# Kernel optimization log

Measured on AMD Instinct MI355X. Metric: run time of the kernel, lower is better.

The kernel has to match this reference:

```python
import jax, jax.numpy as jnp
import numpy as np

NUM_HEADS = 16

def setup_inputs() -> dict:
    key = jax.random.key(0)
    ks = jax.random.split(key, 6)
    B, N, E = 2, 2048, 2048
    QK, V, M = 2048, 2048, 4096
    x = jax.random.normal(ks[0], (B, N, E), dtype=jnp.float32)
    Wq = jax.random.normal(ks[1], (QK, E), dtype=jnp.float32) * 0.02
    k_weight = jax.random.normal(ks[2], (M, QK), dtype=jnp.float32) * 0.05
    v_weight = jax.random.normal(ks[3], (M, V), dtype=jnp.float32) * 0.05
    Wg = jax.random.normal(ks[4], (V, E), dtype=jnp.float32) * 0.02
    Wout = jax.random.normal(ks[5], (E, V), dtype=jnp.float32) * 0.02
    return {"x": x, "Wq": Wq, "k_weight": k_weight, "v_weight": v_weight, "Wg": Wg, "Wout": Wout}

def reference(x, Wq, k_weight, v_weight, Wg, Wout):
    H = NUM_HEADS
    B, N, E = x.shape
    M = k_weight.shape[0]
    # q: [B, N, QK] -> [B, H, N, dk]
    q = jnp.einsum('bne,fe->bnf', x, Wq)
    dk = q.shape[-1] // H
    q = q.reshape(B, N, H, dk).transpose(0, 2, 1, 3)
    # k: [M, QK] -> [H, M, dk]; v: [M, V] -> [H, M, dv]
    k = k_weight.reshape(M, H, dk).transpose(1, 0, 2)
    dv = v_weight.shape[1] // H
    v = v_weight.reshape(M, H, dv).transpose(1, 0, 2)
    scale = jnp.asarray(dk, x.dtype) ** 0.5  # use_scale == 1
    k = k * scale
    v = v * scale
    # non-softmax attention over fixed memory
    energy = jax.nn.silu(jnp.einsum('bhnd,hmd->bhnm', q, k))  # [B,H,N,M]
    out = jnp.einsum('bhnm,hmd->bhnd', energy, v)  # [B,H,N,dv]
    out = out.transpose(0, 2, 1, 3).reshape(B, N, H * dv)
    # output gate (silu)
    gate = jax.nn.silu(jnp.einsum('bne,ve->bnv', x, Wg))
    out = out * gate
    return jnp.einsum('bnv,ev->bne', out, Wout)
```

## Files before the change

### kernel.cpp

```cpp
#include <hip/hip_runtime.h>

typedef __bf16 bf16;
typedef __bf16 bf16x4 __attribute__((ext_vector_type(4)));
typedef __bf16 bf16x8 __attribute__((ext_vector_type(8)));
typedef float f32x4 __attribute__((ext_vector_type(4)));

#define MFMA(a, b, c) __builtin_amdgcn_mfma_f32_16x16x32_bf16(a, b, c, 0, 0, 0)

__device__ __forceinline__ float fast_silu(float x) {
  float e = __builtin_amdgcn_exp2f(x * -1.4426950408889634f);
  return x * __builtin_amdgcn_rcpf(1.f + e);
}

__device__ __forceinline__ void gload_lds16(const void* g, void* l) {
  __builtin_amdgcn_global_load_lds(
      (const __attribute__((address_space(1))) void*)g,
      (__attribute__((address_space(3))) void*)l, 16, 0, 0);
}

__global__ __launch_bounds__(256) void cvt_bf16(const float* __restrict__ in,
                                                bf16* __restrict__ out, int n) {
  int i = (blockIdx.x * 256 + threadIdx.x) * 4;
  if (i >= n) return;
  float4 v = *(const float4*)(in + i);
  bf16x4 o = {(bf16)v.x, (bf16)v.y, (bf16)v.z, (bf16)v.w};
  *(bf16x4*)(out + i) = o;
}

__global__ __launch_bounds__(256) void transpose_v_cvt(const float* __restrict__ v,
                                                       bf16* __restrict__ vt) {
  __shared__ bf16 T[64 * 72];
  const int m0 = blockIdx.x * 64, c0 = blockIdx.y * 64;
  const int tid = threadIdx.x;
  const int tr = tid >> 3;
  const int tc = (tid & 7) << 3;
#pragma unroll
  for (int it = 0; it < 2; it++) {
    int r = tr + it * 32;
    const float* src = v + (long)(m0 + r) * 2048 + c0 + tc;
    float4 a = *(const float4*)src;
    float4 b = *(const float4*)(src + 4);
    bf16x8 t = {(bf16)a.x, (bf16)a.y, (bf16)a.z, (bf16)a.w,
                (bf16)b.x, (bf16)b.y, (bf16)b.z, (bf16)b.w};
    *(bf16x8*)&T[r * 72 + tc] = t;
  }
  __syncthreads();
#pragma unroll
  for (int it = 0; it < 2; it++) {
    int c = tr + it * 32;
    bf16x8 o;
#pragma unroll
    for (int j = 0; j < 8; j++) o[j] = T[(tc + j) * 72 + c];
    *(bf16x8*)(vt + (long)(c0 + c) * 4096 + m0 + tc) = o;
  }
}

template <int MODE, int BM>
__global__ __launch_bounds__(512, 2) void gemm256(const bf16* __restrict__ A,
                                                  const bf16* __restrict__ B,
                                                  const bf16* __restrict__ B2,
                                                  bf16* __restrict__ C1,
                                                  bf16* __restrict__ C2,
                                                  float* __restrict__ Cf, int K, int N) {
  constexpr int MR = BM / 32;
  constexpr int MR2 = MR / 2;
  constexpr int AL = BM / 64;
  __shared__ bf16 As[3][BM * 64];
  __shared__ bf16 Bs[2][256 * 64];

  const int tid = threadIdx.x, wave = tid >> 6, lane = tid & 63;
  const int wr = wave >> 2, wc = wave & 3;
  const int quad = lane >> 4, fr = lane & 15;

  const int id2 = (blockIdx.x & 7) * 32 + (blockIdx.x >> 3);
  const int gx = (MODE == 3) ? (id2 >> 4) : (id2 >> 5);
  const int gy = (MODE == 3) ? (id2 & 15) : (id2 & 31);
  const bool gsel = (MODE == 3) && (gx >= 8);
  const bf16* Bm = gsel ? B2 : B;
  const long bM = (long)gy * BM;
  const long bN = (long)((MODE == 3) ? (gx & 7) : gx) * 256;

  f32x4 acc[MR][4] = {};

  const int srow = tid >> 3;
  const int sblk = (tid & 7) ^ (srow & 7);
  const bf16* Ag = A + (bM + srow) * (long)K + (sblk << 3);
  const bf16* Bg = Bm + (bN + srow) * (long)K + (sblk << 3);
  const int sdst = srow * 64 + ((tid & 7) << 3);

  auto stA = [&](int kt, int sb) {
#pragma unroll
    for (int i = 0; i < AL; i++)
      gload_lds16(Ag + (long)i * 64 * K + kt * 64, &As[sb][sdst + i * 64 * 64]);
  };
  auto stB = [&](int kt, int sb) {
#pragma unroll
    for (int i = 0; i < 4; i++)
      gload_lds16(Bg + (long)i * 64 * K + kt * 64, &Bs[sb][sdst + i * 64 * 64]);
  };
  auto rdA = [&](int ab, int mi, int kk) {
    int row = wr * (BM / 2) + mi * 16 + fr;
    return *(const bf16x8*)&As[ab][row * 64 + (((kk * 4 + quad) ^ (fr & 7)) << 3)];
  };
  auto rdB = [&](int bb, int ni, int kk) {
    int row = wc * 64 + ni * 16 + fr;
    return *(const bf16x8*)&Bs[bb][row * 64 + (((kk * 4 + quad) ^ (fr & 7)) << 3)];
  };

  const int NT = K >> 6;
  stB(0, 0);
  stA(0, 0);
  stA(NT > 1 ? 1 : 0, 1);
  if constexpr (AL == 4)
    asm volatile("s_waitcnt vmcnt(4)" ::: "memory");
  else
    asm volatile("s_waitcnt vmcnt(2)" ::: "memory");
  __builtin_amdgcn_s_barrier();

  for (int kt = 0; kt < NT; ++kt) {
    const int ra = kt % 3, rb = kt & 1;
    bf16x8 bfv[4][2], ah[MR2][2];

    stB(kt + 1 < NT ? kt + 1 : NT - 1, (kt + 1) & 1);
    stA(kt + 2 < NT ? kt + 2 : NT - 1, (kt + 2) % 3);
#pragma unroll
    for (int ni = 0; ni < 4; ni++)
#pragma unroll
      for (int kk = 0; kk < 2; kk++) bfv[ni][kk] = rdB(rb, ni, kk);
#pragma unroll
    for (int mi = 0; mi < MR2; mi++)
#pragma unroll
      for (int kk = 0; kk < 2; kk++) ah[mi][kk] = rdA(ra, mi, kk);
    __builtin_amdgcn_s_barrier();
    __builtin_amdgcn_s_setprio(1);
#pragma unroll
    for (int mi = 0; mi < MR2; mi++)
#pragma unroll
      for (int ni = 0; ni < 2; ni++)
#pragma unroll
        for (int kk = 0; kk < 2; kk++) acc[mi][ni] = MFMA(ah[mi][kk], bfv[ni][kk], acc[mi][ni]);
    __builtin_amdgcn_s_setprio(0);
    __builtin_amdgcn_s_barrier();

    __builtin_amdgcn_s_setprio(1);
#pragma unroll
    for (int mi = 0; mi < MR2; mi++)
#pragma unroll
      for (int ni = 2; ni < 4; ni++)
#pragma unroll
        for (int kk = 0; kk < 2; kk++) acc[mi][ni] = MFMA(ah[mi][kk], bfv[ni][kk], acc[mi][ni]);
    __builtin_amdgcn_s_setprio(0);
    __builtin_amdgcn_s_barrier();

#pragma unroll
    for (int mi = 0; mi < MR2; mi++)
#pragma unroll
      for (int kk = 0; kk < 2; kk++) ah[mi][kk] = rdA(ra, mi + MR2, kk);
    __builtin_amdgcn_s_barrier();
    __builtin_amdgcn_s_setprio(1);
#pragma unroll
    for (int mi = 0; mi < MR2; mi++)
#pragma unroll
      for (int ni = 0; ni < 2; ni++)
#pragma unroll
        for (int kk = 0; kk < 2; kk++)
          acc[mi + MR2][ni] = MFMA(ah[mi][kk], bfv[ni][kk], acc[mi + MR2][ni]);
    __builtin_amdgcn_s_setprio(0);
    __builtin_amdgcn_s_barrier();

    __builtin_amdgcn_s_setprio(1);
#pragma unroll
    for (int mi = 0; mi < MR2; mi++)
#pragma unroll
      for (int ni = 2; ni < 4; ni++)
#pragma unroll
        for (int kk = 0; kk < 2; kk++)
          acc[mi + MR2][ni] = MFMA(ah[mi][kk], bfv[ni][kk], acc[mi + MR2][ni]);
    __builtin_amdgcn_s_setprio(0);
    if constexpr (AL == 4)
      asm volatile("s_waitcnt vmcnt(4)" ::: "memory");
    else
      asm volatile("s_waitcnt vmcnt(2)" ::: "memory");
    __builtin_amdgcn_s_barrier();
  }

#pragma unroll
  for (int mi = 0; mi < MR; mi++)
#pragma unroll
    for (int ni = 0; ni < 4; ni++)
#pragma unroll
      for (int r = 0; r < 4; r++) {
        long row = bM + wr * (BM / 2) + mi * 16 + quad * 4 + r;
        long col = bN + wc * 64 + ni * 16 + fr;
        float v = acc[mi][ni][r];
        if (MODE == 2) {
          Cf[row * (long)N + col] = v;
        } else {
          if (gsel)
            C2[row * (long)N + col] = (bf16)fast_silu(v);
          else
            C1[row * (long)N + col] = (bf16)(v * 11.3137085f);
        }
      }
}

__global__ __launch_bounds__(512, 4) void attn_fused(const bf16* __restrict__ q,
                                                     const bf16* __restrict__ kw,
                                                     const bf16* __restrict__ vt,
                                                     bf16* __restrict__ gate_io) {
  constexpr int E = 2048, M = 4096;
  constexpr float scale = 11.3137085f;
  const int bid = blockIdx.x;
  const int h = ((bid & 7) << 1) | ((bid >> 8) & 1);
  const int sub = (bid >> 3) & 31;
  const int b = sub >> 4, nt = sub & 15;
  const long n0 = (long)b * 2048 + nt * 128;

  const int tid = threadIdx.x, wave = tid >> 6, lane = tid & 63;
  const int quad = lane >> 4, ln = lane & 15;
  const int sw_m = wave & 1, sw_n = wave >> 1;
  const int pw_n = wave & 3, pw_dv = wave >> 2;

  __shared__ bf16 Ks[2][64 * 128];
  __shared__ bf16 Vts[2][128 * 64];
  __shared__ bf16 Ps[128 * 64];

  const bf16* qbase = q + (n0 + sw_n * 32) * E + h * 128;
  bf16x8 qf[2][4];
#pragma unroll
  for (int n2 = 0; n2 < 2; n2++)
#pragma unroll
    for (int ks = 0; ks < 4; ks++)
      qf[n2][ks] = *(const bf16x8*)(qbase + (long)(n2 * 16 + ln) * E + ks * 32 + (quad << 3));

  f32x4 oacc[2][4] = {};

  const bf16* kg = kw + (long)((wave << 3) + quad) * E + h * 128;
  const int ksl_off = (wave << 3) * 128 + lane * 8;
  int kc[2];
#pragma unroll
  for (int i = 0; i < 2; i++) kc[i] = (ln ^ ((wave * 8 + i * 4 + quad) & 15)) << 3;

  const bf16* vg = vt + (long)(h * 128 + (wave << 4) + (lane >> 3)) * M +
                   (((lane & 7) ^ ((lane >> 3) & 7)) << 3);
  const int vsl_off = (wave << 4) * 64 + lane * 8;

  int waddr[2][2];
#pragma unroll
  for (int mt = 0; mt < 2; mt++)
#pragma unroll
    for (int n2 = 0; n2 < 2; n2++) {
      int n = sw_n * 32 + n2 * 16 + ln;
      int mb8 = sw_m * 4 + mt * 2 + (quad >> 1);
      waddr[mt][n2] = n * 64 + ((mb8 ^ (n & 7)) << 3) + ((quad & 1) << 2);
    }

  auto stage = [&](int ms, int sb) {
#pragma unroll
    for (int i = 0; i < 2; i++) {
      gload_lds16(kg + (long)(ms + i * 4) * E + kc[i], &Ks[sb][ksl_off + i * 4 * 128]);
      gload_lds16(vg + ms + (long)i * 8 * M, &Vts[sb][vsl_off + i * 8 * 64]);
    }
  };

  stage(0, 0);
  asm volatile("s_waitcnt vmcnt(0)" ::: "memory");
  __builtin_amdgcn_s_barrier();

  auto body = [&](int m0, int rb, int sb, bool doStage) {
    if (doStage) stage(m0 + 64, sb);

    f32x4 sacc[2][2] = {};
    __builtin_amdgcn_s_setprio(1);
#pragma unroll
    for (int ks = 0; ks < 4; ks++) {
      bf16x8 af[2];
#pragma unroll
      for (int mt = 0; mt < 2; mt++)
        af[mt] = *(const bf16x8*)&Ks[rb][(sw_m * 32 + mt * 16 + ln) * 128 +
                                         (((ks * 4 + quad) ^ ln) << 3)];
#pragma unroll
      for (int mt = 0; mt < 2; mt++)
#pragma unroll
        for (int n2 = 0; n2 < 2; n2++) sacc[mt][n2] = MFMA(af[mt], qf[n2][ks], sacc[mt][n2]);
    }
    __builtin_amdgcn_s_setprio(0);

#pragma unroll
    for (int mt = 0; mt < 2; mt++)
#pragma unroll
      for (int n2 = 0; n2 < 2; n2++) {
        bf16x4 p;
#pragma unroll
        for (int r = 0; r < 4; r++) p[r] = (bf16)fast_silu(sacc[mt][n2][r]);
        *(bf16x4*)&Ps[waddr[mt][n2]] = p;
      }

    asm volatile("s_waitcnt lgkmcnt(0)" ::: "memory");
    __builtin_amdgcn_s_barrier();

#pragma unroll
    for (int ks = 0; ks < 2; ks++) {
      const int so = ((ks * 4 + quad) ^ (ln & 7)) << 3;
      bf16x8 pf[2], vf[4];
#pragma unroll
      for (int n2 = 0; n2 < 2; n2++)
        pf[n2] = *(const bf16x8*)&Ps[(pw_n * 32 + n2 * 16 + ln) * 64 + so];
#pragma unroll
      for (int dt = 0; dt < 4; dt++)
        vf[dt] = *(const bf16x8*)&Vts[rb][(pw_dv * 64 + dt * 16 + ln) * 64 + so];
      __builtin_amdgcn_s_setprio(1);
#pragma unroll
      for (int n2 = 0; n2 < 2; n2++)
#pragma unroll
        for (int dt = 0; dt < 4; dt++) oacc[n2][dt] = MFMA(pf[n2], vf[dt], oacc[n2][dt]);
      __builtin_amdgcn_s_setprio(0);
    }

    asm volatile("s_waitcnt vmcnt(0)" ::: "memory");
    __builtin_amdgcn_s_barrier();
  };

  for (int m0 = 0; m0 < M; m0 += 128) {
    body(m0, 0, 1, true);
    body(m0 + 64, 1, 0, m0 + 128 < M);
  }

  bf16* gio = gate_io + n0 * E + h * 128;
#pragma unroll
  for (int n2 = 0; n2 < 2; n2++)
#pragma unroll
    for (int dt = 0; dt < 4; dt++)
#pragma unroll
      for (int r = 0; r < 4; r++) {
        int n = pw_n * 32 + n2 * 16 + quad * 4 + r;
        int dv = pw_dv * 64 + dt * 16 + ln;
        float g = (float)gio[(long)n * E + dv];
        gio[(long)n * E + dv] = (bf16)(g * oacc[n2][dt][r] * scale);
      }
}

extern "C" void kernel_launch(void* const* d_in, const int* in_sizes, int n_in,
                              void* d_out, int out_size, void* d_ws, size_t ws_size,
                              hipStream_t stream) {
  const float* x = (const float*)d_in[0];
  const float* Wq = (const float*)d_in[1];
  const float* kw = (const float*)d_in[2];
  const float* vw = (const float*)d_in[3];
  const float* Wg = (const float*)d_in[4];
  const float* Wout = (const float*)d_in[5];
  float* out = (float*)d_out;
  bf16* ws = (bf16*)d_ws;

  bf16* S0 = ws;
  bf16* S1 = ws + 8388608;
  bf16* S2 = ws + 16777216;
  bf16* S3 = ws + 25165824;
  bf16* S4 = ws + 33554432;
  bf16* Wgb = S1 + 4194304;

  cvt_bf16<<<8192, 256, 0, stream>>>(x, S0, 8388608);
  cvt_bf16<<<4096, 256, 0, stream>>>(Wq, S1, 4194304);
  cvt_bf16<<<4096, 256, 0, stream>>>(Wg, Wgb, 4194304);
  transpose_v_cvt<<<dim3(64, 32), 256, 0, stream>>>(vw, S2);
  gemm256<3, 256><<<256, 512, 0, stream>>>(S0, S1, Wgb, S3, S4, (float*)nullptr, 2048, 2048);
  cvt_bf16<<<8192, 256, 0, stream>>>(kw, S0, 8388608);
  attn_fused<<<512, 512, 0, stream>>>(S3, S0, S2, S4);
  cvt_bf16<<<4096, 256, 0, stream>>>(Wout, S1, 4194304);
  gemm256<2, 128><<<256, 512, 0, stream>>>(S4, S1, (const bf16*)nullptr, (bf16*)nullptr,
                                           (bf16*)nullptr, out, 2048, 2048);
}
```

Before: 478.3 us.

## Interleave GEMM global-to-LDS loads across MFMA phases and merge conversion kernels

In the bf16 GEMM, the prefetch loads for the next B and A tiles are no longer issued all at the start of each k-iteration. They are now spread across the four MFMA phases, with extra barriers, so memory traffic overlaps with tensor-core work instead of arriving in one burst. Separately, the four fp32→bf16 conversion and transpose launches are merged into one kernel, and the k_weight and Wout conversions into a second, which cuts kernel launch overhead. The extra barriers could add synchronisation cost, and Wout is now converted earlier, before the attention kernel runs.

```diff
diff --git a/kernel.cpp b/kernel.cpp
--- a/kernel.cpp
+++ b/kernel.cpp
@@ -18,41 +18,65 @@
       (__attribute__((address_space(3))) void*)l, 16, 0, 0);
 }
 
-__global__ __launch_bounds__(256) void cvt_bf16(const float* __restrict__ in,
-                                                bf16* __restrict__ out, int n) {
-  int i = (blockIdx.x * 256 + threadIdx.x) * 4;
-  if (i >= n) return;
+__device__ __forceinline__ void cvt4(const float* __restrict__ in,
+                                     bf16* __restrict__ out, int i) {
   float4 v = *(const float4*)(in + i);
   bf16x4 o = {(bf16)v.x, (bf16)v.y, (bf16)v.z, (bf16)v.w};
   *(bf16x4*)(out + i) = o;
 }
 
-__global__ __launch_bounds__(256) void transpose_v_cvt(const float* __restrict__ v,
-                                                       bf16* __restrict__ vt) {
+__global__ __launch_bounds__(256) void prep1(const float* __restrict__ x,
+                                             const float* __restrict__ Wq,
+                                             const float* __restrict__ Wg,
+                                             const float* __restrict__ vw,
+                                             bf16* __restrict__ xb,
+                                             bf16* __restrict__ Wqb,
+                                             bf16* __restrict__ Wgb,
+                                             bf16* __restrict__ vt) {
   __shared__ bf16 T[64 * 72];
-  const int m0 = blockIdx.x * 64, c0 = blockIdx.y * 64;
-  const int tid = threadIdx.x;
-  const int tr = tid >> 3;
-  const int tc = (tid & 7) << 3;
-#pragma unroll
-  for (int it = 0; it < 2; it++) {
-    int r = tr + it * 32;
-    const float* src = v + (long)(m0 + r) * 2048 + c0 + tc;
-    float4 a = *(const float4*)src;
-    float4 b = *(const float4*)(src + 4);
-    bf16x8 t = {(bf16)a.x, (bf16)a.y, (bf16)a.z, (bf16)a.w,
-                (bf16)b.x, (bf16)b.y, (bf16)b.z, (bf16)b.w};
-    *(bf16x8*)&T[r * 72 + tc] = t;
+  const int b = blockIdx.x, tid = threadIdx.x;
+  if (b < 8192) {
+    cvt4(x, xb, (b * 256 + tid) * 4);
+  } else if (b < 12288) {
+    cvt4(Wq, Wqb, ((b - 8192) * 256 + tid) * 4);
+  } else if (b < 16384) {
+    cvt4(Wg, Wgb, ((b - 12288) * 256 + tid) * 4);
+  } else {
+    const int bid2 = b - 16384;
+    const int m0 = (bid2 & 63) * 64, c0 = (bid2 >> 6) * 64;
+    const int tr = tid >> 3;
+    const int tc = (tid & 7) << 3;
+#pragma unroll
+    for (int it = 0; it < 2; it++) {
+      int r = tr + it * 32;
+      const float* src = vw + (long)(m0 + r) * 2048 + c0 + tc;
+      float4 a = *(const float4*)src;
+      float4 bb = *(const float4*)(src + 4);
+      bf16x8 t = {(bf16)a.x, (bf16)a.y, (bf16)a.z, (bf16)a.w,
+                  (bf16)bb.x, (bf16)bb.y, (bf16)bb.z, (bf16)bb.w};
+      *(bf16x8*)&T[r * 72 + tc] = t;
+    }
+    __syncthreads();
+#pragma unroll
+    for (int it = 0; it < 2; it++) {
+      int c = tr + it * 32;
+      bf16x8 o;
+#pragma unroll
+      for (int j = 0; j < 8; j++) o[j] = T[(tc + j) * 72 + c];
+      *(bf16x8*)(vt + (long)(c0 + c) * 4096 + m0 + tc) = o;
+    }
   }
-  __syncthreads();
-#pragma unroll
-  for (int it = 0; it < 2; it++) {
-    int c = tr + it * 32;
-    bf16x8 o;
-#pragma unroll
-    for (int j = 0; j < 8; j++) o[j] = T[(tc + j) * 72 + c];
-    *(bf16x8*)(vt + (long)(c0 + c) * 4096 + m0 + tc) = o;
-  }
+}
+
+__global__ __launch_bounds__(256) void prep2(const float* __restrict__ kw,
+                                             const float* __restrict__ Wout,
+                                             bf16* __restrict__ kwb,
+                                             bf16* __restrict__ Woutb) {
+  const int b = blockIdx.x, tid = threadIdx.x;
+  if (b < 8192)
+    cvt4(kw, kwb, (b * 256 + tid) * 4);
+  else
+    cvt4(Wout, Woutb, ((b - 8192) * 256 + tid) * 4);
 }
 
 template <int MODE, int BM>
@@ -64,7 +88,7 @@
                                                   float* __restrict__ Cf, int K, int N) {
   constexpr int MR = BM / 32;
   constexpr int MR2 = MR / 2;
-  constexpr int AL = BM / 64;
+  constexpr int NA = BM / 64;
   __shared__ bf16 As[3][BM * 64];
   __shared__ bf16 Bs[2][256 * 64];
 
@@ -88,15 +112,11 @@
   const bf16* Bg = Bm + (bN + srow) * (long)K + (sblk << 3);
   const int sdst = srow * 64 + ((tid & 7) << 3);
 
-  auto stA = [&](int kt, int sb) {
-#pragma unroll
-    for (int i = 0; i < AL; i++)
-      gload_lds16(Ag + (long)i * 64 * K + kt * 64, &As[sb][sdst + i * 64 * 64]);
-  };
-  auto stB = [&](int kt, int sb) {
-#pragma unroll
-    for (int i = 0; i < 4; i++)
-      gload_lds16(Bg + (long)i * 64 * K + kt * 64, &Bs[sb][sdst + i * 64 * 64]);
+  auto stA = [&](int kt, int sb, int i) {
+    gload_lds16(Ag + (long)i * 64 * K + kt * 64, &As[sb][sdst + i * 64 * 64]);
+  };
+  auto stB = [&](int kt, int sb, int i) {
+    gload_lds16(Bg + (long)i * 64 * K + kt * 64, &Bs[sb][sdst + i * 64 * 64]);
   };
   auto rdA = [&](int ab, int mi, int kk) {
     int row = wr * (BM / 2) + mi * 16 + fr;
@@ -108,10 +128,13 @@
   };
 
   const int NT = K >> 6;
-  stB(0, 0);
-  stA(0, 0);
-  stA(NT > 1 ? 1 : 0, 1);
-  if constexpr (AL == 4)
+#pragma unroll
+  for (int i = 0; i < 4; i++) stB(0, 0, i);
+#pragma unroll
+  for (int i = 0; i < NA; i++) stA(0, 0, i);
+#pragma unroll
+  for (int i = 0; i < NA; i++) stA(NT > 1 ? 1 : 0, 1, i);
+  if constexpr (NA == 4)
     asm volatile("s_waitcnt vmcnt(4)" ::: "memory");
   else
     asm volatile("s_waitcnt vmcnt(2)" ::: "memory");
@@ -119,10 +142,10 @@
 
   for (int kt = 0; kt < NT; ++kt) {
     const int ra = kt % 3, rb = kt & 1;
+    const int ktB = kt + 1 < NT ? kt + 1 : NT - 1, bb = (kt + 1) & 1;
+    const int ktA = kt + 2 < NT ? kt + 2 : NT - 1, ab2 = (kt + 2) % 3;
     bf16x8 bfv[4][2], ah[MR2][2];
 
-    stB(kt + 1 < NT ? kt + 1 : NT - 1, (kt + 1) & 1);
-    stA(kt + 2 < NT ? kt + 2 : NT - 1, (kt + 2) % 3);
 #pragma unroll
     for (int ni = 0; ni < 4; ni++)
 #pragma unroll
@@ -131,6 +154,8 @@
     for (int mi = 0; mi < MR2; mi++)
 #pragma unroll
       for (int kk = 0; kk < 2; kk++) ah[mi][kk] = rdA(ra, mi, kk);
+    stB(ktB, bb, 0);
+    stB(ktB, bb, 1);
     __builtin_amdgcn_s_barrier();
     __builtin_amdgcn_s_setprio(1);
 #pragma unroll
@@ -142,6 +167,9 @@
     __builtin_amdgcn_s_setprio(0);
     __builtin_amdgcn_s_barrier();
 
+    stB(ktB, bb, 2);
+    stB(ktB, bb, 3);
+    __builtin_amdgcn_s_barrier();
     __builtin_amdgcn_s_setprio(1);
 #pragma unroll
     for (int mi = 0; mi < MR2; mi++)
@@ -156,6 +184,9 @@
     for (int mi = 0; mi < MR2; mi++)
 #pragma unroll
       for (int kk = 0; kk < 2; kk++) ah[mi][kk] = rdA(ra, mi + MR2, kk);
+    stA(ktA, ab2, 0);
+    if constexpr (NA == 4) stA(ktA, ab2, 1);
+    else stA(ktA, ab2, 1);
     __builtin_amdgcn_s_barrier();
     __builtin_amdgcn_s_setprio(1);
 #pragma unroll
@@ -168,6 +199,11 @@
     __builtin_amdgcn_s_setprio(0);
     __builtin_amdgcn_s_barrier();
 
+    if constexpr (NA == 4) {
+      stA(ktA, ab2, 2);
+      stA(ktA, ab2, 3);
+    }
+    __builtin_amdgcn_s_barrier();
     __builtin_amdgcn_s_setprio(1);
 #pragma unroll
     for (int mi = 0; mi < MR2; mi++)
@@ -177,7 +213,7 @@
         for (int kk = 0; kk < 2; kk++)
           acc[mi + MR2][ni] = MFMA(ah[mi][kk], bfv[ni][kk], acc[mi + MR2][ni]);
     __builtin_amdgcn_s_setprio(0);
-    if constexpr (AL == 4)
+    if constexpr (NA == 4)
       asm volatile("s_waitcnt vmcnt(4)" ::: "memory");
     else
       asm volatile("s_waitcnt vmcnt(2)" ::: "memory");
@@ -359,14 +395,10 @@
   bf16* S4 = ws + 33554432;
   bf16* Wgb = S1 + 4194304;
 
-  cvt_bf16<<<8192, 256, 0, stream>>>(x, S0, 8388608);
-  cvt_bf16<<<4096, 256, 0, stream>>>(Wq, S1, 4194304);
-  cvt_bf16<<<4096, 256, 0, stream>>>(Wg, Wgb, 4194304);
-  transpose_v_cvt<<<dim3(64, 32), 256, 0, stream>>>(vw, S2);
+  prep1<<<18432, 256, 0, stream>>>(x, Wq, Wg, vw, S0, S1, Wgb, S2);
   gemm256<3, 256><<<256, 512, 0, stream>>>(S0, S1, Wgb, S3, S4, (float*)nullptr, 2048, 2048);
-  cvt_bf16<<<8192, 256, 0, stream>>>(kw, S0, 8388608);
+  prep2<<<12288, 256, 0, stream>>>(kw, Wout, S0, S1);
   attn_fused<<<512, 512, 0, stream>>>(S3, S0, S2, S4);
-  cvt_bf16<<<4096, 256, 0, stream>>>(Wout, S1, 4194304);
   gemm256<2, 128><<<256, 512, 0, stream>>>(S4, S1, (const bf16*)nullptr, (bf16*)nullptr,
                                            (bf16*)nullptr, out, 2048, 2048);
 }
```

After: 440.6 us. 7.9% less time.
